# Kernel optimization log

Hardware: AMD Instinct MI355X
Metric: run time of the kernel (lower is better)

Reference implementation:

```python
import jax, jax.numpy as jnp
import numpy as np

N = 100800          # anchors for YOLOv5 @ 1280px: 3*(160^2+80^2+40^2)
NC = 80             # COCO classes
CONF_THRES = 0.4
IOU_THRES = 0.45
MAX_DET = 1000
MAX_NMS = 4096      # candidate cap before IoU (ultralytics uses 30000; reduced for KxK IoU memory)
MAX_WH = 7680.0     # per-class box offset (agnostic=False)


def setup_inputs() -> dict:
    key = jax.random.key(0)
    k1, k2, k3, k4 = jax.random.split(key, 4)
    xy = jax.random.uniform(k1, (1, N, 2), jnp.float32) * 1280.0   # box centers
    wh = jax.random.uniform(k2, (1, N, 2), jnp.float32) * 200.0 + 2.0  # box sizes
    obj = jax.random.uniform(k3, (1, N, 1), jnp.float32)           # objectness
    cls = jax.random.uniform(k4, (1, N, NC), jnp.float32)          # class scores
    pred = jnp.concatenate([xy, wh, obj, cls], axis=-1)            # [1, N, 85]
    return {"pred": pred}


def _xywh2xyxy(b):
    xy, wh = b[:, :2], b[:, 2:4]
    return jnp.concatenate([xy - wh * 0.5, xy + wh * 0.5], axis=-1)


def _nms(pred):
    p = pred[0]                                   # [N, 85] (module returns image 0)
    cls_conf = p[:, 5:] * p[:, 4:5]               # conf = obj * cls
    conf = jnp.max(cls_conf, axis=-1)             # best-class confidence [N]
    cls = jnp.argmax(cls_conf, axis=-1)           # best-class index [N]
    box = _xywh2xyxy(p[:, :4])                    # [N, 4] xyxy

    # candidate filter (conf > thres) + cap to top MAX_NMS by confidence
    scores = jnp.where(conf > CONF_THRES, conf, -jnp.inf)
    top_s, idx = jax.lax.top_k(scores, MAX_NMS)   # sorted descending
    b = box[idx]                                  # [K, 4]
    c = cls[idx]                                  # [K]
    valid = top_s > CONF_THRES                    # [K]

    # per-class NMS: offset boxes by class index so classes never overlap
    ob = b + (c.astype(b.dtype) * MAX_WH)[:, None]
    area = (ob[:, 2] - ob[:, 0]) * (ob[:, 3] - ob[:, 1])
    lt = jnp.maximum(ob[:, None, :2], ob[None, :, :2])
    rb = jnp.minimum(ob[:, None, 2:], ob[None, :, 2:])
    whi = jnp.clip(rb - lt, 0.0)
    inter = whi[..., 0] * whi[..., 1]             # [K, K]
    iou = inter / (area[:, None] + area[None, :] - inter + 1e-9)

    # greedy NMS: box j is suppressed if a kept, higher-scoring box i overlaps it
    upper = jnp.triu(jnp.ones((MAX_NMS, MAX_NMS), bool), 1)
    sup_mat = jax.lax.stop_gradient((iou > IOU_THRES) & upper)

    def body(i, keep):
        return keep & ~(sup_mat[i] & keep[i])

    keep = jax.lax.stop_gradient(jax.lax.fori_loop(0, MAX_NMS, body, valid))

    # top max_det kept detections, padded with zeros -> fixed [MAX_DET, 6]
    fscore = jnp.where(keep, top_s, -jnp.inf)
    fs, fi = jax.lax.top_k(fscore, MAX_DET)
    out = jnp.concatenate(
        [b[fi], top_s[fi][:, None], c[fi].astype(b.dtype)[:, None]], axis=-1
    )                                             # [MAX_DET, 6] = x1,y1,x2,y2,conf,cls
    return jnp.where((fs > CONF_THRES)[:, None], out, 0.0)


def reference(pred):
    return _nms(pred)
```

## Files before the change

### kernel.cpp

```cpp
#include <hip/hip_runtime.h>
#include <stdint.h>

#pragma clang fp contract(off)

#define N_ANCH 100800
#define ROWLEN 85
#define NCLS 80
#define CONF_T 0.4f
#define IOU_T 0.45f
#define MAXNMS 4096
#define MAXDET 1000
#define NBINS 4096
#define MAX_WH_F 7680.0f
#define SROWS 132
#define SCORE_BLKS ((N_ANCH + SROWS - 1) / SROWS)
#define POISON32 0xAAAAAAAAu


__device__ __forceinline__ unsigned long long aload64(const unsigned long long* p) {
  return __hip_atomic_load(p, __ATOMIC_RELAXED, __HIP_MEMORY_SCOPE_AGENT);
}
__device__ __forceinline__ void astore64(unsigned long long* p, unsigned long long v) {
  __hip_atomic_store(p, v, __ATOMIC_RELAXED, __HIP_MEMORY_SCOPE_AGENT);
}
__device__ __forceinline__ unsigned aload32(const unsigned* p) {
  return __hip_atomic_load(p, __ATOMIC_RELAXED, __HIP_MEMORY_SCOPE_AGENT);
}
__device__ __forceinline__ void astore32(unsigned* p, unsigned v) {
  __hip_atomic_store(p, v, __ATOMIC_RELAXED, __HIP_MEMORY_SCOPE_AGENT);
}

__device__ __forceinline__ unsigned key_anchor(unsigned long long key) {
  return (~(unsigned)(key >> 8)) & 0x1FFFFu;
}
__device__ __forceinline__ unsigned key_cls(unsigned long long key) {
  return (unsigned)key & 0xFFu;
}

__global__ __launch_bounds__(256) void score_kernel(
    const float* __restrict__ pred, float* __restrict__ confArr,
    unsigned char* __restrict__ clsArr, unsigned short* __restrict__ binArr,
    unsigned* __restrict__ hist, unsigned* __restrict__ base,
    unsigned* __restrict__ meta) {
  __shared__ float s[SROWS * ROWLEN];
  __shared__ unsigned s_scan[4];
  __shared__ unsigned s_last;
  const int tid = threadIdx.x;
  const int wid = tid >> 6, lane = tid & 63;

  {
    const float4* p4 = (const float4*)pred;
    float4* s4 = (float4*)s;
    const int NV = SROWS * ROWLEN / 4;
    const size_t g0 = (size_t)blockIdx.x * NV;
    const size_t gmax = (size_t)N_ANCH * ROWLEN / 4;
    for (int v = tid; v < NV; v += 256) {
      size_t g = g0 + v;
      if (g < gmax) s4[v] = p4[g];
    }
  }
  __syncthreads();

  if (tid < SROWS) {
    int n = blockIdx.x * SROWS + tid;
    if (n < N_ANCH) {
      const float* row = s + tid * ROWLEN;
      float obj = row[4];
      float best = row[5] * obj;
      int bc = 0;
      for (int i = 1; i < NCLS; ++i) {
        float v = row[5 + i] * obj;
        if (v > best) { best = v; bc = i; }
      }
      confArr[n] = best;
      clsArr[n] = (unsigned char)bc;
      unsigned short bo = 0;
      if (best > CONF_T) {
        int b = (int)(best * 4096.0f);
        if (b > NBINS - 1) b = NBINS - 1;
        bo = (unsigned short)b;
        atomicAdd(&hist[b], 1u);
      }
      binArr[n] = bo;
    }
  }

  __syncthreads();
  if (tid == 0) {
    unsigned ret = __hip_atomic_fetch_add(&meta[8], 1u, __ATOMIC_RELAXED,
                                          __HIP_MEMORY_SCOPE_AGENT);
    s_last = (ret == POISON32 + (unsigned)(SCORE_BLKS - 1)) ? 1u : 0u;
  }
  __syncthreads();
  if (s_last == 0) return;

  unsigned hv[16];
  unsigned ssum = 0;
#pragma unroll
  for (int k = 0; k < 16; ++k) {
    hv[k] = aload32(&hist[NBINS - 1 - (tid * 16 + k)]) - POISON32;
    ssum += hv[k];
  }
  unsigned incl = ssum;
  for (int d = 1; d < 64; d <<= 1) {
    unsigned v = __shfl_up(incl, d);
    if (lane >= d) incl += v;
  }
  if (lane == 63) s_scan[wid] = incl;
  __syncthreads();
  if (tid == 0) {
    unsigned acc = 0;
    for (int w = 0; w < 4; ++w) { unsigned t = s_scan[w]; s_scan[w] = acc; acc += t; }
  }
  __syncthreads();
  unsigned e = s_scan[wid] + (incl - ssum);
#pragma unroll
  for (int k = 0; k < 16; ++k) {
    int b = NBINS - 1 - (tid * 16 + k);
    base[b] = e;
    if (e <= (unsigned)MAXNMS && e + hv[k] > (unsigned)MAXNMS) {
      meta[0] = (unsigned)(b + 1);
      meta[1] = e;
    }
    e += hv[k];
  }
  if (tid == 255) meta[2] = e;
}

__global__ __launch_bounds__(256) void gather_kernel(
    const float* __restrict__ confArr, const unsigned short* __restrict__ binArr,
    const unsigned char* __restrict__ clsArr,
    const unsigned* __restrict__ base, unsigned* __restrict__ cnt,
    const unsigned* __restrict__ meta, unsigned long long* __restrict__ cand) {
  int v = blockIdx.x * 256 + threadIdx.x;
  if (v >= N_ANCH / 4) return;
  ushort4 b4 = ((const ushort4*)binArr)[v];
  const unsigned Bcut = meta[0];
  int n0 = v * 4;
#pragma unroll
  for (int k = 0; k < 4; ++k) {
    unsigned b = (k == 0) ? b4.x : (k == 1) ? b4.y : (k == 2) ? b4.z : b4.w;
    if (b && b >= Bcut) {
      int n = n0 + k;
      unsigned r = atomicAdd(&cnt[b], 1u) - POISON32;
      unsigned long long key =
          ((unsigned long long)__float_as_uint(confArr[n]) << 32) |
          ((unsigned long long)((~(unsigned)n) & 0x1FFFFu) << 8) |
          (unsigned long long)clsArr[n];
      cand[base[b] + r] = key;
    }
  }
}

__global__ __launch_bounds__(64) void rank_kernel(
    const unsigned long long* __restrict__ cand,
    const unsigned* __restrict__ base, const unsigned* __restrict__ cnt,
    const unsigned* __restrict__ meta, unsigned* __restrict__ clsCnt,
    unsigned long long* __restrict__ clsKeys, unsigned* __restrict__ clsSlots) {
  const unsigned Bcut = meta[0];
  const unsigned total =
      Bcut ? meta[1] : (meta[2] > (unsigned)MAXNMS ? (unsigned)MAXNMS : meta[2]);
  unsigned t = blockIdx.x * 64 + threadIdx.x;
  if (t >= total) return;
  unsigned long long key = cand[t];
  float conf = __uint_as_float((unsigned)(key >> 32));
  int b = (int)(conf * 4096.0f);
  if (b > NBINS - 1) b = NBINS - 1;
  unsigned bs = base[b], ct = cnt[b] - POISON32;
  unsigned r = 0;
  for (unsigned j = 0; j < ct; ++j) r += (cand[bs + j] > key) ? 1u : 0u;
  unsigned slot = bs + r;
  unsigned c = key_cls(key);
  unsigned idx = atomicAdd(&clsCnt[c], 1u) - POISON32;
  if (idx < 128) {
    clsKeys[(size_t)c * 128 + idx] = key;
    clsSlots[(size_t)c * 128 + idx] = slot;
  }
}

__global__ __launch_bounds__(256) void class_kernel(
    const float* __restrict__ pred,
    const unsigned* __restrict__ clsCnt,
    const unsigned long long* __restrict__ clsKeys,
    const unsigned* __restrict__ clsSlots,
    unsigned* __restrict__ meta,
    unsigned* __restrict__ keep32, unsigned long long* __restrict__ sortedKey,
    float* __restrict__ out) {
  __shared__ unsigned long long s_mkey[128];
  __shared__ unsigned s_mslot[128];
  __shared__ float4 s_obox[128];
  __shared__ unsigned long long s_okey[128];
  __shared__ unsigned s_oslot[128];
  __shared__ unsigned s_scan[4];
  __shared__ unsigned s_last;
  __shared__ unsigned short s_kept[MAXDET];
  __shared__ unsigned s_tot;

  const int tid = threadIdx.x;
  const int wid = tid >> 6, lane = tid & 63;
  const int c = blockIdx.x;

  int K = (int)(clsCnt[c] - POISON32);
  if (K > 128) K = 128;

  if (tid < K) {
    s_mkey[tid] = clsKeys[(size_t)c * 128 + tid];
    s_mslot[tid] = clsSlots[(size_t)c * 128 + tid];
  }
  __syncthreads();

  if (K > 0) {
    if (tid < K) {
      unsigned myslot = s_mslot[tid];
      unsigned ord = 0;
      for (int j = 0; j < K; ++j) ord += (s_mslot[j] < myslot) ? 1u : 0u;
      unsigned long long key = s_mkey[tid];
      unsigned a = key_anchor(key);
      const float* row = pred + (size_t)a * ROWLEN;
      float bx = row[0], by = row[1], bw = row[2], bh = row[3];
      float x1 = bx - bw * 0.5f, y1 = by - bh * 0.5f;
      float x2 = bx + bw * 0.5f, y2 = by + bh * 0.5f;
      float off = (float)c * MAX_WH_F;
      s_obox[ord] = make_float4(x1 + off, y1 + off, x2 + off, y2 + off);
      s_okey[ord] = key;
      s_oslot[ord] = myslot;
    }
    __syncthreads();
    if (wid == 0) {
      const int nch = (K + 63) >> 6;
      float ox1[2], oy1[2], ox2[2], oy2[2];
#pragma unroll
      for (int q = 0; q < 2; ++q) {
        ox1[q] = oy1[q] = ox2[q] = oy2[q] = 0.f;
        int j = q * 64 + lane;
        if (q < nch && j < K) {
          float4 bb = s_obox[j];
          ox1[q] = bb.x; oy1[q] = bb.y; ox2[q] = bb.z; oy2[q] = bb.w;
        }
      }
      unsigned long long cm00 = 0ull, cm01 = 0ull, cm10 = 0ull, cm11 = 0ull;
#pragma unroll
      for (int qi = 0; qi < 2; ++qi) {
        if (qi < nch) {
          int lim = K - qi * 64; if (lim > 64) lim = 64;
          for (int li = 0; li < lim; ++li) {
            float bx1 = __shfl(qi ? ox1[1] : ox1[0], li);
            float by1 = __shfl(qi ? oy1[1] : oy1[0], li);
            float bx2 = __shfl(qi ? ox2[1] : ox2[0], li);
            float by2 = __shfl(qi ? oy2[1] : oy2[0], li);
            float areai = (bx2 - bx1) * (by2 - by1);
            int i = qi * 64 + li;
            unsigned long long bit = (1ull << li);
#pragma unroll
            for (int q = 0; q < 2; ++q) {
              if (q < nch) {
                int j = q * 64 + lane;
                float ltx = fmaxf(bx1, ox1[q]);
                float lty = fmaxf(by1, oy1[q]);
                float rbx = fminf(bx2, ox2[q]);
                float rby = fminf(by2, oy2[q]);
                float iw = fmaxf(rbx - ltx, 0.f);
                float ih = fmaxf(rby - lty, 0.f);
                float inter = iw * ih;
                float areaj = (ox2[q] - ox1[q]) * (oy2[q] - oy1[q]);
                float iou = inter / (areai + areaj - inter + 1e-9f);
                bool sup = (iou > IOU_T) && (i < j) && (j < K);
                if (sup) {
                  if (q == 0) { if (qi == 0) cm00 |= bit; else cm01 |= bit; }
                  else       { if (qi == 0) cm10 |= bit; else cm11 |= bit; }
                }
              }
            }
          }
        }
      }
      unsigned long long vm0, vm1, km0, km1;
      {
        int r0 = K;      vm0 = (r0 >= 64) ? ~0ull : ((1ull << r0) - 1ull);
        int r1 = K - 64; vm1 = (r1 >= 64) ? ~0ull
                                          : ((r1 <= 0) ? 0ull : ((1ull << r1) - 1ull));
        km0 = vm0; km1 = vm1;
      }
      for (int it = 0; it < 200; ++it) {
        unsigned long long s0 = cm00 & km0;
        if (nch > 1) s0 |= cm01 & km1;
        unsigned long long b0 = __ballot(s0 == 0ull) & vm0;
        unsigned long long b1 = km1;
        if (nch > 1) {
          unsigned long long s1 = (cm10 & km0) | (cm11 & km1);
          b1 = __ballot(s1 == 0ull) & vm1;
        }
        bool same = (b0 == km0) && (b1 == km1);
        km0 = b0; km1 = b1;
        if (same) break;
      }
#pragma unroll
      for (int q = 0; q < 2; ++q) {
        int j = q * 64 + lane;
        if (q < nch && j < K) {
          unsigned slot = s_oslot[j];
          astore32(&keep32[slot],
                   (unsigned)(((q == 0 ? km0 : km1) >> lane) & 1ull));
          astore64(&sortedKey[slot], s_okey[j]);
        }
      }
    }
  }

  __syncthreads();
  if (tid == 0) {
    unsigned ret = __hip_atomic_fetch_add(&meta[9], 1u, __ATOMIC_RELAXED,
                                          __HIP_MEMORY_SCOPE_AGENT);
    s_last = (ret == POISON32 + (unsigned)(NCLS - 1)) ? 1u : 0u;
  }
  __syncthreads();
  if (s_last == 0) return;

  unsigned flags[16];
  unsigned fsum = 0;
#pragma unroll
  for (int k = 0; k < 16; ++k) {
    flags[k] = (aload32(&keep32[tid * 16 + k]) == 1u) ? 1u : 0u;
    fsum += flags[k];
  }
  unsigned incl = fsum;
  for (int d = 1; d < 64; d <<= 1) {
    unsigned v = __shfl_up(incl, d);
    if (lane >= d) incl += v;
  }
  if (lane == 63) s_scan[wid] = incl;
  __syncthreads();
  if (tid == 0) {
    unsigned acc = 0;
    for (int w = 0; w < 4; ++w) { unsigned t = s_scan[w]; s_scan[w] = acc; acc += t; }
    s_tot = acc;
  }
  __syncthreads();
  unsigned rank = s_scan[wid] + (incl - fsum);
#pragma unroll
  for (int k = 0; k < 16; ++k) {
    if (flags[k]) {
      if (rank < MAXDET) s_kept[rank] = (unsigned short)(tid * 16 + k);
      rank++;
    }
  }
  __syncthreads();
  unsigned tot = s_tot;
  for (int r = tid; r < MAXDET; r += 256) {
    float* o = out + (size_t)r * 6;
    if (r < (int)tot) {
      int slot = s_kept[r];
      unsigned long long key = aload64(&sortedKey[slot]);
      unsigned a = key_anchor(key);
      float conf = __uint_as_float((unsigned)(key >> 32));
      const float* row = pred + (size_t)a * ROWLEN;
      float bx = row[0], by = row[1], bw = row[2], bh = row[3];
      o[0] = bx - bw * 0.5f; o[1] = by - bh * 0.5f;
      o[2] = bx + bw * 0.5f; o[3] = by + bh * 0.5f;
      o[4] = conf; o[5] = (float)key_cls(key);
    } else {
      o[0] = 0.f; o[1] = 0.f; o[2] = 0.f;
      o[3] = 0.f; o[4] = 0.f; o[5] = 0.f;
    }
  }
}

extern "C" void kernel_launch(void* const* d_in, const int* in_sizes, int n_in,
                              void* d_out, int out_size, void* d_ws, size_t ws_size,
                              hipStream_t stream) {
  (void)in_sizes; (void)n_in; (void)out_size; (void)ws_size;
  const float* pred = (const float*)d_in[0];
  float* out = (float*)d_out;
  char* ws = (char*)d_ws;

  unsigned* hist = (unsigned*)(ws + 0);
  unsigned* cnt = (unsigned*)(ws + 16384);
  unsigned* keep32 = (unsigned*)(ws + 32768);
  unsigned* meta = (unsigned*)(ws + 49152);
  unsigned* base = (unsigned*)(ws + 49280);
  unsigned long long* cand = (unsigned long long*)(ws + 65664);
  unsigned long long* sortedKey = (unsigned long long*)(ws + 98432);
  float* confArr = (float*)(ws + 131200);
  unsigned char* clsArr = (unsigned char*)(ws + 534400);
  unsigned short* binArr = (unsigned short*)(ws + 635200);
  unsigned* clsCnt = (unsigned*)(ws + 836800);
  unsigned long long* clsKeys = (unsigned long long*)(ws + 837376);
  unsigned* clsSlots = (unsigned*)(ws + 919296);

  score_kernel<<<SCORE_BLKS, 256, 0, stream>>>(pred, confArr, clsArr, binArr,
                                               hist, base, meta);
  gather_kernel<<<(N_ANCH / 4 + 255) / 256, 256, 0, stream>>>(
      confArr, binArr, clsArr, base, cnt, meta, cand);
  rank_kernel<<<MAXNMS / 64, 64, 0, stream>>>(cand, base, cnt, meta, clsCnt,
                                              clsKeys, clsSlots);
  class_kernel<<<NCLS, 256, 0, stream>>>(pred, clsCnt, clsKeys, clsSlots, meta,
                                         keep32, sortedKey, out);
}
```

Measured before the change: 122.5 us.

## Fuse gather and rank kernels using last-block-done pattern with LDS candidate staging

New measurement: 125.7 us. 2.6% more time.

```diff
diff --git a/kernel.cpp b/kernel.cpp
--- a/kernel.cpp
+++ b/kernel.cpp
@@ -15,6 +15,9 @@
 #define SROWS 132
 #define SCORE_BLKS ((N_ANCH + SROWS - 1) / SROWS)
 #define POISON32 0xAAAAAAAAu
+#define GR_THREADS 1024
+#define GR_ITEMS (N_ANCH / 4)
+#define GR_BLKS ((GR_ITEMS + GR_THREADS - 1) / GR_THREADS)
 
 
 __device__ __forceinline__ unsigned long long aload64(const unsigned long long* p) {
@@ -127,54 +130,67 @@
   if (tid == 255) meta[2] = e;
 }
 
-__global__ __launch_bounds__(256) void gather_kernel(
+__global__ __launch_bounds__(GR_THREADS) void gather_rank_kernel(
     const float* __restrict__ confArr, const unsigned short* __restrict__ binArr,
     const unsigned char* __restrict__ clsArr,
     const unsigned* __restrict__ base, unsigned* __restrict__ cnt,
-    const unsigned* __restrict__ meta, unsigned long long* __restrict__ cand) {
-  int v = blockIdx.x * 256 + threadIdx.x;
-  if (v >= N_ANCH / 4) return;
-  ushort4 b4 = ((const ushort4*)binArr)[v];
+    unsigned* __restrict__ meta, unsigned long long* __restrict__ cand,
+    unsigned* __restrict__ clsCnt, unsigned long long* __restrict__ clsKeys,
+    unsigned* __restrict__ clsSlots) {
+  __shared__ unsigned long long s_cand[MAXNMS];
+  __shared__ unsigned s_last;
+  const int tid = threadIdx.x;
+  const int v = blockIdx.x * GR_THREADS + tid;
   const unsigned Bcut = meta[0];
-  int n0 = v * 4;
-#pragma unroll
-  for (int k = 0; k < 4; ++k) {
-    unsigned b = (k == 0) ? b4.x : (k == 1) ? b4.y : (k == 2) ? b4.z : b4.w;
-    if (b && b >= Bcut) {
-      int n = n0 + k;
-      unsigned r = atomicAdd(&cnt[b], 1u) - POISON32;
-      unsigned long long key =
-          ((unsigned long long)__float_as_uint(confArr[n]) << 32) |
-          ((unsigned long long)((~(unsigned)n) & 0x1FFFFu) << 8) |
-          (unsigned long long)clsArr[n];
-      cand[base[b] + r] = key;
-    }
-  }
-}
-
-__global__ __launch_bounds__(64) void rank_kernel(
-    const unsigned long long* __restrict__ cand,
-    const unsigned* __restrict__ base, const unsigned* __restrict__ cnt,
-    const unsigned* __restrict__ meta, unsigned* __restrict__ clsCnt,
-    unsigned long long* __restrict__ clsKeys, unsigned* __restrict__ clsSlots) {
-  const unsigned Bcut = meta[0];
+
+  if (v < GR_ITEMS) {
+    ushort4 b4 = ((const ushort4*)binArr)[v];
+    int n0 = v * 4;
+#pragma unroll
+    for (int k = 0; k < 4; ++k) {
+      unsigned b = (k == 0) ? b4.x : (k == 1) ? b4.y : (k == 2) ? b4.z : b4.w;
+      if (b && b >= Bcut) {
+        int n = n0 + k;
+        unsigned r = atomicAdd(&cnt[b], 1u) - POISON32;
+        unsigned long long key =
+            ((unsigned long long)__float_as_uint(confArr[n]) << 32) |
+            ((unsigned long long)((~(unsigned)n) & 0x1FFFFu) << 8) |
+            (unsigned long long)clsArr[n];
+        astore64(&cand[base[b] + r], key);
+      }
+    }
+  }
+
+  __syncthreads();
+  if (tid == 0) {
+    unsigned ret = __hip_atomic_fetch_add(&meta[11], 1u, __ATOMIC_RELAXED,
+                                          __HIP_MEMORY_SCOPE_AGENT);
+    s_last = (ret == POISON32 + (unsigned)(GR_BLKS - 1)) ? 1u : 0u;
+  }
+  __syncthreads();
+  if (s_last == 0) return;
+
   const unsigned total =
       Bcut ? meta[1] : (meta[2] > (unsigned)MAXNMS ? (unsigned)MAXNMS : meta[2]);
-  unsigned t = blockIdx.x * 64 + threadIdx.x;
-  if (t >= total) return;
-  unsigned long long key = cand[t];
-  float conf = __uint_as_float((unsigned)(key >> 32));
-  int b = (int)(conf * 4096.0f);
-  if (b > NBINS - 1) b = NBINS - 1;
-  unsigned bs = base[b], ct = cnt[b] - POISON32;
-  unsigned r = 0;
-  for (unsigned j = 0; j < ct; ++j) r += (cand[bs + j] > key) ? 1u : 0u;
-  unsigned slot = bs + r;
-  unsigned c = key_cls(key);
-  unsigned idx = atomicAdd(&clsCnt[c], 1u) - POISON32;
-  if (idx < 128) {
-    clsKeys[(size_t)c * 128 + idx] = key;
-    clsSlots[(size_t)c * 128 + idx] = slot;
+  for (unsigned i = tid; i < total; i += GR_THREADS)
+    s_cand[i] = aload64(&cand[i]);
+  __syncthreads();
+
+  for (unsigned t = tid; t < total; t += GR_THREADS) {
+    unsigned long long key = s_cand[t];
+    float conf = __uint_as_float((unsigned)(key >> 32));
+    int b = (int)(conf * 4096.0f);
+    if (b > NBINS - 1) b = NBINS - 1;
+    unsigned bs = base[b], ct = aload32(&cnt[b]) - POISON32;
+    unsigned r = 0;
+    for (unsigned j = 0; j < ct; ++j) r += (s_cand[bs + j] > key) ? 1u : 0u;
+    unsigned slot = bs + r;
+    unsigned c = key_cls(key);
+    unsigned idx = atomicAdd(&clsCnt[c], 1u) - POISON32;
+    if (idx < 128) {
+      clsKeys[(size_t)c * 128 + idx] = key;
+      clsSlots[(size_t)c * 128 + idx] = slot;
+    }
   }
 }
 
@@ -389,10 +405,9 @@
 
   score_kernel<<<SCORE_BLKS, 256, 0, stream>>>(pred, confArr, clsArr, binArr,
                                                hist, base, meta);
-  gather_kernel<<<(N_ANCH / 4 + 255) / 256, 256, 0, stream>>>(
-      confArr, binArr, clsArr, base, cnt, meta, cand);
-  rank_kernel<<<MAXNMS / 64, 64, 0, stream>>>(cand, base, cnt, meta, clsCnt,
-                                              clsKeys, clsSlots);
+  gather_rank_kernel<<<GR_BLKS, GR_THREADS, 0, stream>>>(
+      confArr, binArr, clsArr, base, cnt, meta, cand, clsCnt, clsKeys,
+      clsSlots);
   class_kernel<<<NCLS, 256, 0, stream>>>(pred, clsCnt, clsKeys, clsSlots, meta,
                                          keep32, sortedKey, out);
 }
```
